# Optimization experiments

Hardware: AMD Instinct MI355X
Metric: run time of the kernel (lower is better)

## Reference

```python
import jax, jax.numpy as jnp
import numpy as np

EMBED_DIM = 1024
N_HEADS = 16
HEAD_SIZE = EMBED_DIM // N_HEADS
SCALE = HEAD_SIZE ** -0.5


def setup_inputs() -> dict:
    key = jax.random.key(0)
    ks = jax.random.split(key, 11)
    B, Tq, Tk, C = 4, 1024, 1024, EMBED_DIM
    std = 0.02
    return {
        "q": jax.random.normal(ks[0], (B, Tq, C), jnp.float32),
        "k": jax.random.normal(ks[1], (B, Tk, C), jnp.float32),
        "v": jax.random.normal(ks[2], (B, Tk, C), jnp.float32),
        "Wq": jax.random.normal(ks[3], (C, C), jnp.float32) * std,
        "bq": jnp.zeros((C,), jnp.float32),
        "Wk": jax.random.normal(ks[4], (C, C), jnp.float32) * std,
        "bk": jnp.zeros((C,), jnp.float32),
        "Wv": jax.random.normal(ks[5], (C, C), jnp.float32) * std,
        "bv": jnp.zeros((C,), jnp.float32),
        "Wo": jax.random.normal(ks[6], (C, C), jnp.float32) * std,
        "bo": jnp.zeros((C,), jnp.float32),
    }


def reference(q, k, v, Wq, bq, Wk, bk, Wv, bv, Wo, bo):
    b, t, c = q.shape
    # linear projections (torch Linear: x @ W.T + b)
    qp = q @ Wq.T + bq            # [b, tq, c]
    kp = k @ Wk.T + bk            # [b, tk, c]
    vp = v @ Wv.T + bv            # [b, tk, c]
    # split heads: [b, h, t, d]
    qh = qp.reshape(b, t, N_HEADS, HEAD_SIZE).transpose(0, 2, 1, 3)
    kh = kp.reshape(b, kp.shape[1], N_HEADS, HEAD_SIZE).transpose(0, 2, 1, 3)
    vh = vp.reshape(b, vp.shape[1], N_HEADS, HEAD_SIZE).transpose(0, 2, 1, 3)
    # scaled dot-product attention
    scores = jnp.einsum('bhqd,bhkd->bhqk', qh, kh) * SCALE
    weights = jax.nn.softmax(scores, axis=-1)
    attn = jnp.einsum('bhqk,bhkd->bhqd', weights, vh)
    attn = attn.transpose(0, 2, 1, 3).reshape(b, t, c)
    out = attn @ Wo.T + bo
    return out
```

## Files before the change

### kernel.cpp

```cpp
#include <hip/hip_runtime.h>
#include <stdint.h>

typedef unsigned short u16;
typedef unsigned int   u32;
typedef __bf16 bf16;
typedef bf16  bf16x2 __attribute__((ext_vector_type(2)));
typedef bf16  bf16x8 __attribute__((ext_vector_type(8)));
typedef float f32x4  __attribute__((ext_vector_type(4)));

#define AS1 __attribute__((address_space(1)))
#define AS3 __attribute__((address_space(3)))


__device__ __forceinline__ u32 pk2(float lo, float hi) {
  bf16x2 t;
  t[0] = (bf16)lo;
  t[1] = (bf16)hi;
  return __builtin_bit_cast(u32, t);
}

__device__ __forceinline__ u16 b1(float f) {
  bf16 t = (bf16)f;
  return __builtin_bit_cast(u16, t);
}

__device__ __forceinline__ void gload_lds16(const void* src, void* dst) {
  __builtin_amdgcn_global_load_lds((const AS1 void*)src, (AS3 void*)dst, 16, 0, 0);
}

__device__ __forceinline__ bf16x8 fragS(const char* lds, int row, int kbyte) {
  return *(const bf16x8*)(lds + row * 128 + (kbyte ^ ((row & 7) << 4)));
}


__global__ __launch_bounds__(256) void cvt_w(
    const float* wq, const float* wk, const float* wv, const float* wo,
    u16* wqb, u16* wkb, u16* wvb, u16* wob)
{
  const float* src; u16* dst;
  switch (blockIdx.y) {
    case 0: src = wq; dst = wqb; break;
    case 1: src = wk; dst = wkb; break;
    case 2: src = wv; dst = wvb; break;
    default: src = wo; dst = wob; break;
  }
  const int n4 = 262144;
  int stride = gridDim.x * blockDim.x;
  for (int i = blockIdx.x * blockDim.x + threadIdx.x; i < n4; i += stride) {
    float4 f = ((const float4*)src)[i];
    uint2 o;
    o.x = pk2(f.x, f.y);
    o.y = pk2(f.z, f.w);
    ((uint2*)dst)[i] = o;
  }
}


template<int NC>
__device__ __forceinline__ void stageSw(const u16* gtile, char* lds, int tid)
{
  int w = tid >> 6, lane = tid & 63;
  int rr = lane >> 3;
  int cb = (lane & 7) << 4;
  #pragma unroll
  for (int i = 0; i < NC; ++i) {
    int c = i * 4 + w;
    int r = c * 8 + rr;
    gload_lds16((const char*)(gtile + r * 1024) + (cb ^ (rr << 4)), lds + c * 1024);
  }
}

__device__ __forceinline__ void loadA64(const float* gA, int tid,
                                        float4* pa, float4* pb)
{
  int r0 = tid >> 3, c8 = (tid & 7) << 3;
  #pragma unroll
  for (int i = 0; i < 2; ++i) {
    const float* p = gA + (i * 32 + r0) * 1024 + c8;
    pa[i] = *(const float4*)p;
    pb[i] = *(const float4*)(p + 4);
  }
}

__device__ __forceinline__ void writeA64(char* lds, int tid,
                                         const float4* pa, const float4* pb)
{
  int r0 = tid >> 3, cb = (tid & 7) << 4;
  #pragma unroll
  for (int i = 0; i < 2; ++i) {
    int r = i * 32 + r0;
    uint4 o;
    o.x = pk2(pa[i].x, pa[i].y);
    o.y = pk2(pa[i].z, pa[i].w);
    o.z = pk2(pb[i].x, pb[i].y);
    o.w = pk2(pb[i].z, pb[i].w);
    *(uint4*)(lds + r * 128 + (cb ^ ((r & 7) << 4))) = o;
  }
}

__device__ __forceinline__ void mfma_64x128(const char* As, const char* Bs,
                                            f32x4 acc[2][4], int lane,
                                            int wr, int wc)
{
  int g = lane >> 4;
  #pragma unroll
  for (int ks = 0; ks < 2; ++ks) {
    int kb = ks * 64 + (g << 4);
    bf16x8 af[2], bfr[4];
    #pragma unroll
    for (int m = 0; m < 2; ++m) af[m]  = fragS(As, wr * 32 + m * 16 + (lane & 15), kb);
    #pragma unroll
    for (int n = 0; n < 4; ++n) bfr[n] = fragS(Bs, wc * 64 + n * 16 + (lane & 15), kb);
    #pragma unroll
    for (int m = 0; m < 2; ++m)
      #pragma unroll
      for (int n = 0; n < 4; ++n)
        acc[m][n] = __builtin_amdgcn_mfma_f32_16x16x32_bf16(af[m], bfr[n], acc[m][n], 0, 0, 0);
  }
}


__global__ __launch_bounds__(256, 3) void proj_gemm(
    const float* qf, const float* kf, const float* vf,
    const u16* wqb, const u16* wkb, const u16* wvb,
    const float* bq, const float* bk, const float* bv,
    u16* qh, u16* kh, u16* vt)
{
  __shared__ alignas(16) char As[2][8192];
  __shared__ alignas(16) char Bs[2][16384];
  int tid = threadIdx.x;
  int bi = blockIdx.x & 63, bj = blockIdx.x >> 6;
  int z = blockIdx.z;
  const float* A = (z == 0) ? qf : (z == 1) ? kf : vf;
  const u16* W = (z == 0) ? wqb : (z == 1) ? wkb : wvb;
  const float* bias = (z == 0) ? bq : (z == 1) ? bk : bv;
  u16* dst = (z == 0) ? qh : (z == 1) ? kh : vt;

  int lane = tid & 63;
  int wr = (tid >> 7) & 1, wc = (tid >> 6) & 1;

  float4 pa[2], pb[2];
  loadA64(A + bi * 65536, tid, pa, pb);
  stageSw<4>(W + bj * 131072, Bs[0], tid);
  writeA64(As[0], tid, pa, pb);
  loadA64(A + bi * 65536 + 64, tid, pa, pb);
  __syncthreads();

  f32x4 acc[2][4] = {};
  int cur = 0;
  for (int kt = 0; kt < 16; ++kt) {
    if (kt < 15) {
      stageSw<4>(W + bj * 131072 + (kt + 1) * 64, Bs[cur ^ 1], tid);
      writeA64(As[cur ^ 1], tid, pa, pb);
      if (kt < 14)
        loadA64(A + bi * 65536 + (kt + 2) * 64, tid, pa, pb);
    }
    mfma_64x128(As[cur], Bs[cur], acc, lane, wr, wc);
    __syncthreads();
    cur ^= 1;
  }

  int rbase = bi * 64 + wr * 32 + ((lane >> 4) << 2);
  int cbase = bj * 128 + wc * 64;
  #pragma unroll
  for (int n = 0; n < 4; ++n) {
    int col = cbase + n * 16 + (lane & 15);
    float bsv = bias[col];
    int h = col >> 6, d = col & 63;
    #pragma unroll
    for (int m = 0; m < 2; ++m) {
      #pragma unroll
      for (int r = 0; r < 4; ++r) {
        int R = rbase + m * 16 + r;
        int b = R >> 10, t = R & 1023;
        u16 val = b1(acc[m][n][r] + bsv);
        if (z < 2) dst[(((b * 16 + h) * 1024 + t) << 6) + d] = val;
        else       dst[(((b * 16 + h) * 64 + d) << 10) + t] = val;
      }
    }
  }
}


__global__ __launch_bounds__(256, 3) void out_gemm(
    const u16* attn, const u16* wob, const float* bo, float* out)
{
  __shared__ alignas(16) char As[2][8192];
  __shared__ alignas(16) char Bs[2][16384];
  int tid = threadIdx.x;
  int bi = blockIdx.x & 63, bj = blockIdx.x >> 6;

  int lane = tid & 63;
  int wr = (tid >> 7) & 1, wc = (tid >> 6) & 1;

  stageSw<2>(attn + bi * 65536, As[0], tid);
  stageSw<4>(wob + bj * 131072, Bs[0], tid);
  __syncthreads();

  f32x4 acc[2][4] = {};
  int cur = 0;
  for (int kt = 0; kt < 16; ++kt) {
    if (kt < 15) {
      stageSw<2>(attn + bi * 65536  + (kt + 1) * 64, As[cur ^ 1], tid);
      stageSw<4>(wob  + bj * 131072 + (kt + 1) * 64, Bs[cur ^ 1], tid);
    }
    mfma_64x128(As[cur], Bs[cur], acc, lane, wr, wc);
    __syncthreads();
    cur ^= 1;
  }

  int rbase = bi * 64 + wr * 32 + ((lane >> 4) << 2);
  int cbase = bj * 128 + wc * 64;
  #pragma unroll
  for (int n = 0; n < 4; ++n) {
    int col = cbase + n * 16 + (lane & 15);
    float bsv = bo[col];
    #pragma unroll
    for (int m = 0; m < 2; ++m) {
      #pragma unroll
      for (int r = 0; r < 4; ++r) {
        int R = rbase + m * 16 + r;
        out[R * 1024 + col] = acc[m][n][r] + bsv;
      }
    }
  }
}


__global__ __launch_bounds__(256, 2) void attn_fwd(
    const u16* qh, const u16* kh, const u16* vt, u16* attnb)
{
  __shared__ alignas(16) u16 Ks[64 * 72];
  __shared__ alignas(16) u16 Vs[64 * 72];
  __shared__ alignas(16) u16 Pl[4][16 * 72];

  const float SC = 0.125f;
  const float RTHR = 64.0f;

  int tid = threadIdx.x, lane = tid & 63, w = tid >> 6;
  int g = lane >> 4;
  int q0 = blockIdx.x << 6;
  int bh = blockIdx.y;
  const u16* qbase = qh + bh * 65536;
  const u16* kbase = kh + bh * 65536;
  const u16* vbase = vt + bh * 65536;

  bf16x8 qf[2];
  {
    int qrow = q0 + w * 16 + (lane & 15);
    const u16* p = qbase + qrow * 64 + (g << 3);
    qf[0] = *(const bf16x8*)p;
    qf[1] = *(const bf16x8*)(p + 32);
  }

  f32x4 ot[4] = {};
  float m_r = -3.0e38f, l_r = 0.f;

  int sr = tid >> 2;
  int sj = (tid & 3) << 4;
  u16* pw = Pl[w];
  int prow = (lane & 15) * 72;

  const u16* ksrc0 = kbase + sr * 64 + sj;
  const u16* vsrc0 = vbase + sr * 1024 + sj;

  bf16x8 kr0, kr1, vr0, vr1;
  kr0 = *(const bf16x8*)(ksrc0);
  kr1 = *(const bf16x8*)(ksrc0 + 8);
  vr0 = *(const bf16x8*)(vsrc0);
  vr1 = *(const bf16x8*)(vsrc0 + 8);

  for (int kv0 = 0; kv0 < 1024; kv0 += 64) {
    *(bf16x8*)(Ks + sr * 72 + sj)     = kr0;
    *(bf16x8*)(Ks + sr * 72 + sj + 8) = kr1;
    *(bf16x8*)(Vs + sr * 72 + sj)     = vr0;
    *(bf16x8*)(Vs + sr * 72 + sj + 8) = vr1;
    __syncthreads();

    if (kv0 < 960) {
      const u16* kn = ksrc0 + (kv0 + 64) * 64;
      const u16* vn = vsrc0 + (kv0 + 64);
      kr0 = *(const bf16x8*)(kn);
      kr1 = *(const bf16x8*)(kn + 8);
      vr0 = *(const bf16x8*)(vn);
      vr1 = *(const bf16x8*)(vn + 8);
    }

    f32x4 sc[4] = {};
    #pragma unroll
    for (int ks = 0; ks < 2; ++ks) {
      #pragma unroll
      for (int m = 0; m < 4; ++m) {
        bf16x8 kf = *(const bf16x8*)(Ks + (m * 16 + (lane & 15)) * 72 + ks * 32 + g * 8);
        sc[m] = __builtin_amdgcn_mfma_f32_16x16x32_bf16(kf, qf[ks], sc[m], 0, 0, 0);
      }
    }

    float vmax = -3.0e38f;
    #pragma unroll
    for (int m = 0; m < 4; ++m)
      #pragma unroll
      for (int r = 0; r < 4; ++r)
        vmax = fmaxf(vmax, sc[m][r]);
    vmax = fmaxf(vmax, __shfl_xor(vmax, 16, 64));
    vmax = fmaxf(vmax, __shfl_xor(vmax, 32, 64));

    if (!__all(vmax - m_r <= RTHR)) {
      float mnew = fmaxf(m_r, vmax);
      float fac = __expf((m_r - mnew) * SC);
      l_r *= fac;
      #pragma unroll
      for (int dm = 0; dm < 4; ++dm) ot[dm] *= fac;
      m_r = mnew;
    }
    float nm = -m_r * SC;

    float psum = 0.f;
    u32 pp[4][2];
    #pragma unroll
    for (int m = 0; m < 4; ++m) {
      float p0 = __expf(fmaf(sc[m][0], SC, nm));
      float p1 = __expf(fmaf(sc[m][1], SC, nm));
      float p2 = __expf(fmaf(sc[m][2], SC, nm));
      float p3 = __expf(fmaf(sc[m][3], SC, nm));
      psum += (p0 + p1) + (p2 + p3);
      pp[m][0] = pk2(p0, p1);
      pp[m][1] = pk2(p2, p3);
    }
    psum += __shfl_xor(psum, 16, 64);
    psum += __shfl_xor(psum, 32, 64);
    l_r += psum;

    #pragma unroll
    for (int m = 0; m < 4; ++m) {
      u32* d = (u32*)(pw + prow + m * 16 + (g << 2));
      d[0] = pp[m][0];
      d[1] = pp[m][1];
    }

    #pragma unroll
    for (int ks = 0; ks < 2; ++ks) {
      bf16x8 pf = *(const bf16x8*)(pw + prow + ks * 32 + g * 8);
      #pragma unroll
      for (int dm = 0; dm < 4; ++dm) {
        bf16x8 vf = *(const bf16x8*)(Vs + (dm * 16 + (lane & 15)) * 72 + ks * 32 + g * 8);
        ot[dm] = __builtin_amdgcn_mfma_f32_16x16x32_bf16(vf, pf, ot[dm], 0, 0, 0);
      }
    }
    __syncthreads();
  }

  float inv = 1.0f / l_r;
  int b = bh >> 4, h = bh & 15;
  int tok = (b << 10) + q0 + w * 16 + (lane & 15);
  u16* obase = attnb + tok * 1024 + h * 64;
  #pragma unroll
  for (int dm = 0; dm < 4; ++dm) {
    int d0 = dm * 16 + (g << 2);
    u32* d = (u32*)(obase + d0);
    d[0] = pk2(ot[dm][0] * inv, ot[dm][1] * inv);
    d[1] = pk2(ot[dm][2] * inv, ot[dm][3] * inv);
  }
}


extern "C" void kernel_launch(void* const* d_in, const int* in_sizes, int n_in,
                              void* d_out, int out_size, void* d_ws, size_t ws_size,
                              hipStream_t stream)
{
  const float* q  = (const float*)d_in[0];
  const float* k  = (const float*)d_in[1];
  const float* v  = (const float*)d_in[2];
  const float* Wq = (const float*)d_in[3];
  const float* bq = (const float*)d_in[4];
  const float* Wk = (const float*)d_in[5];
  const float* bk = (const float*)d_in[6];
  const float* Wv = (const float*)d_in[7];
  const float* bv = (const float*)d_in[8];
  const float* Wo = (const float*)d_in[9];
  const float* bo = (const float*)d_in[10];
  float* out = (float*)d_out;

  u16* ws  = (u16*)d_ws;
  u16* wqb = ws;
  u16* wkb = wqb + (1u << 20);
  u16* wvb = wkb + (1u << 20);
  u16* wob = wvb + (1u << 20);
  u16* qhb = wob + (1u << 20);
  u16* khb = qhb + (4u << 20);
  u16* vtb = khb + (4u << 20);
  u16* atb = vtb + (4u << 20);

  cvt_w<<<dim3(256, 4, 1), 256, 0, stream>>>(Wq, Wk, Wv, Wo, wqb, wkb, wvb, wob);
  proj_gemm<<<dim3(512, 1, 3), 256, 0, stream>>>(q, k, v, wqb, wkb, wvb,
                                                 bq, bk, bv, qhb, khb, vtb);
  attn_fwd<<<dim3(16, 64, 1), 256, 0, stream>>>(qhb, khb, vtb, atb);
  out_gemm<<<dim3(512, 1, 1), 256, 0, stream>>>(atb, wob, bo, out);
}
```

Before: 220.5 us.

## Triple-buffer projection and output GEMMs with explicit vmcnt waits

Both GEMM kernels move from a double-buffered LDS pipeline with __syncthreads to a three-stage ring buffer that prefetches two K-tiles ahead. Barriers are replaced by fine-grained s_waitcnt vmcnt counts plus sched_barrier-wrapped s_barrier, so loads still in flight are not drained every iteration. The fp32 A operand in proj_gemm is also register double-buffered. The larger LDS footprint lowers the launch-bounds occupancy hint from 3 to 2 blocks per CU, and the hand-counted vmcnt values must match the exact number of loads issued.

```diff
diff --git a/kernel.cpp b/kernel.cpp
--- a/kernel.cpp
+++ b/kernel.cpp
@@ -10,6 +10,11 @@
 
 #define AS1 __attribute__((address_space(1)))
 #define AS3 __attribute__((address_space(3)))
+
+#define VMW(N) asm volatile("s_waitcnt vmcnt(" #N ")" ::: "memory")
+#define LGW0   asm volatile("s_waitcnt lgkmcnt(0)" ::: "memory")
+#define SCB    __builtin_amdgcn_sched_barrier(0)
+#define BAR    __builtin_amdgcn_s_barrier()
 
 
 __device__ __forceinline__ u32 pk2(float lo, float hi) {
@@ -120,14 +125,14 @@
 }
 
 
-__global__ __launch_bounds__(256, 3) void proj_gemm(
+__global__ __launch_bounds__(256, 2) void proj_gemm(
     const float* qf, const float* kf, const float* vf,
     const u16* wqb, const u16* wkb, const u16* wvb,
     const float* bq, const float* bk, const float* bv,
     u16* qh, u16* kh, u16* vt)
 {
-  __shared__ alignas(16) char As[2][8192];
-  __shared__ alignas(16) char Bs[2][16384];
+  __shared__ alignas(16) char As[3][8192];
+  __shared__ alignas(16) char Bs[3][16384];
   int tid = threadIdx.x;
   int bi = blockIdx.x & 63, bj = blockIdx.x >> 6;
   int z = blockIdx.z;
@@ -138,26 +143,34 @@
 
   int lane = tid & 63;
   int wr = (tid >> 7) & 1, wc = (tid >> 6) & 1;
-
-  float4 pa[2], pb[2];
-  loadA64(A + bi * 65536, tid, pa, pb);
-  stageSw<4>(W + bj * 131072, Bs[0], tid);
-  writeA64(As[0], tid, pa, pb);
-  loadA64(A + bi * 65536 + 64, tid, pa, pb);
-  __syncthreads();
+  const float* Ab = A + bi * 65536;
+  const u16*  Wb = W + bj * 131072;
+
+  float4 pa[2][2], pb[2][2];
+  loadA64(Ab, tid, pa[0], pb[0]);
+  stageSw<4>(Wb, Bs[0], tid);
+  loadA64(Ab + 64, tid, pa[1], pb[1]);
+  stageSw<4>(Wb + 64, Bs[1], tid);
+  writeA64(As[0], tid, pa[0], pb[0]);
+  loadA64(Ab + 128, tid, pa[0], pb[0]);
+  VMW(12);
+  LGW0;
+  SCB; BAR; SCB;
 
   f32x4 acc[2][4] = {};
-  int cur = 0;
-  for (int kt = 0; kt < 16; ++kt) {
-    if (kt < 15) {
-      stageSw<4>(W + bj * 131072 + (kt + 1) * 64, Bs[cur ^ 1], tid);
-      writeA64(As[cur ^ 1], tid, pa, pb);
-      if (kt < 14)
-        loadA64(A + bi * 65536 + (kt + 2) * 64, tid, pa, pb);
-    }
-    mfma_64x128(As[cur], Bs[cur], acc, lane, wr, wc);
-    __syncthreads();
-    cur ^= 1;
+  #pragma unroll
+  for (int t = 0; t < 16; ++t) {
+    if (t + 1 < 16) writeA64(As[(t + 1) % 3], tid, pa[(t + 1) & 1], pb[(t + 1) & 1]);
+    if (t + 3 < 16) loadA64(Ab + (t + 3) * 64, tid, pa[(t + 3) & 1], pb[(t + 3) & 1]);
+    if (t + 2 < 16) stageSw<4>(Wb + (t + 2) * 64, Bs[(t + 2) % 3], tid);
+    mfma_64x128(As[t % 3], Bs[t % 3], acc, lane, wr, wc);
+    if (t < 15) {
+      if (t <= 12)      VMW(8);
+      else if (t == 13) VMW(4);
+      else              VMW(0);
+      LGW0;
+      SCB; BAR; SCB;
+    }
   }
 
   int rbase = bi * 64 + wr * 32 + ((lane >> 4) << 2);
@@ -182,31 +195,39 @@
 }
 
 
-__global__ __launch_bounds__(256, 3) void out_gemm(
+__global__ __launch_bounds__(256, 2) void out_gemm(
     const u16* attn, const u16* wob, const float* bo, float* out)
 {
-  __shared__ alignas(16) char As[2][8192];
-  __shared__ alignas(16) char Bs[2][16384];
+  __shared__ alignas(16) char As[3][8192];
+  __shared__ alignas(16) char Bs[3][16384];
   int tid = threadIdx.x;
   int bi = blockIdx.x & 63, bj = blockIdx.x >> 6;
 
   int lane = tid & 63;
   int wr = (tid >> 7) & 1, wc = (tid >> 6) & 1;
-
-  stageSw<2>(attn + bi * 65536, As[0], tid);
-  stageSw<4>(wob + bj * 131072, Bs[0], tid);
-  __syncthreads();
+  const u16* Ab = attn + bi * 65536;
+  const u16* Wb = wob + bj * 131072;
+
+  stageSw<2>(Ab, As[0], tid);
+  stageSw<4>(Wb, Bs[0], tid);
+  stageSw<2>(Ab + 64, As[1], tid);
+  stageSw<4>(Wb + 64, Bs[1], tid);
+  VMW(6);
+  SCB; BAR; SCB;
 
   f32x4 acc[2][4] = {};
-  int cur = 0;
-  for (int kt = 0; kt < 16; ++kt) {
-    if (kt < 15) {
-      stageSw<2>(attn + bi * 65536  + (kt + 1) * 64, As[cur ^ 1], tid);
-      stageSw<4>(wob  + bj * 131072 + (kt + 1) * 64, Bs[cur ^ 1], tid);
-    }
-    mfma_64x128(As[cur], Bs[cur], acc, lane, wr, wc);
-    __syncthreads();
-    cur ^= 1;
+  #pragma unroll
+  for (int t = 0; t < 16; ++t) {
+    if (t + 2 < 16) {
+      stageSw<2>(Ab + (t + 2) * 64, As[(t + 2) % 3], tid);
+      stageSw<4>(Wb + (t + 2) * 64, Bs[(t + 2) % 3], tid);
+    }
+    mfma_64x128(As[t % 3], Bs[t % 3], acc, lane, wr, wc);
+    if (t < 15) {
+      if (t <= 13) VMW(6);
+      else         VMW(0);
+      SCB; BAR; SCB;
+    }
   }
 
   int rbase = bi * 64 + wr * 32 + ((lane >> 4) << 2);
```

Result: no change. 221.5 us (+0.5%).
